# Kernel optimization log

Measured on AMD Instinct MI355X. Metric: run time of the kernel, lower is better.

## Reference

```python
import jax, jax.numpy as jnp
import numpy as np

B, S, D, H = 4, 2048, 1024, 16
DK = D // H  # 64


def setup_inputs() -> dict:
    key = jax.random.key(0)
    ks = jax.random.split(key, 7)
    scale = 1.0 / np.sqrt(D)
    q = jax.random.normal(ks[0], (B, S, D), dtype=jnp.float32)
    k = jax.random.normal(ks[1], (B, S, D), dtype=jnp.float32)
    v = jax.random.normal(ks[2], (B, S, D), dtype=jnp.float32)
    # causal mask, broadcastable to [B, H, S, S]
    mask = jnp.tril(jnp.ones((S, S), dtype=jnp.int32))[None, None, :, :]
    Wq = jax.random.normal(ks[3], (D, D), dtype=jnp.float32) * scale
    Wk = jax.random.normal(ks[4], (D, D), dtype=jnp.float32) * scale
    Wv = jax.random.normal(ks[5], (D, D), dtype=jnp.float32) * scale
    Wo = jax.random.normal(ks[6], (D, D), dtype=jnp.float32) * scale
    return {"q": q, "k": k, "v": v, "mask": mask,
            "Wq": Wq, "Wk": Wk, "Wv": Wv, "Wo": Wo}


def reference(q, k, v, mask, Wq, Wk, Wv, Wo):
    # nn.Linear(bias=False): y = x @ W.T
    query = jnp.einsum('bsd,ed->bse', q, Wq).reshape(B, S, H, DK).transpose(0, 2, 1, 3)
    key_ = jnp.einsum('bsd,ed->bse', k, Wk).reshape(B, S, H, DK).transpose(0, 2, 1, 3)
    value = jnp.einsum('bsd,ed->bse', v, Wv).reshape(B, S, H, DK).transpose(0, 2, 1, 3)
    scores = jnp.einsum('bhqd,bhkd->bhqk', query, key_) / jnp.sqrt(jnp.float32(DK))
    scores = jnp.where(mask == 0, -jnp.inf, scores)
    probs = jax.nn.softmax(scores, axis=-1)
    x = jnp.einsum('bhqk,bhkd->bhqd', probs, value)  # [B,H,S,DK]
    x = x.transpose(0, 2, 1, 3).reshape(B, S, D)
    return jnp.einsum('bsd,ed->bse', x, Wo)
```

## Files before the change

### kernel.cpp

```cpp
#include <hip/hip_runtime.h>
#include <hip/hip_bf16.h>

constexpr int Bn = 4, Sn = 2048, Dn = 1024, Hn = 16, DKn = 64;
constexpr int Mrows = Bn * Sn;
constexpr int NQB = Sn / 64;

typedef __attribute__((ext_vector_type(8))) short short8;
typedef __attribute__((ext_vector_type(4))) float f32x4;
typedef __attribute__((ext_vector_type(4))) unsigned int u32x4;

#define DEV __device__ __forceinline__

DEV unsigned short f2bf(float f) {
    unsigned u = __builtin_bit_cast(unsigned, f);
    u += 0x7FFFu + ((u >> 16) & 1u);
    return (unsigned short)(u >> 16);
}
DEV unsigned pk2(float a, float b) {
    __hip_bfloat162 h = __float22bfloat162_rn(float2{a, b});
    unsigned u;
    __builtin_memcpy(&u, &h, 4);
    return u;
}
DEV float exp2a(float x) {
    float r;
    asm("v_exp_f32 %0, %1" : "=v"(r) : "v"(x));
    return r;
}

__global__ __launch_bounds__(256) void cvt_w(const float* __restrict__ W0,
                                             const float* __restrict__ W1,
                                             const float* __restrict__ W2,
                                             const float* __restrict__ W3,
                                             unsigned short* __restrict__ Out) {
    const float* src = blockIdx.y == 0 ? W0
                     : blockIdx.y == 1 ? W1
                     : blockIdx.y == 2 ? W2 : W3;
    size_t off = ((size_t)blockIdx.x * 256 + threadIdx.x) * 8;
    const float4* s = (const float4*)(src + off);
    float4 a = s[0], b = s[1];
    u32x4 p = {pk2(a.x, a.y), pk2(a.z, a.w), pk2(b.x, b.y), pk2(b.z, b.w)};
    *(u32x4*)(Out + (size_t)blockIdx.y * (Dn * Dn) + off) = p;
}

template <bool ABF16, bool BBF16, bool OUTF32>
DEV void gemm_body(const void* __restrict__ Ap, const void* __restrict__ Bw,
                   void* __restrict__ Out) {
    __shared__ alignas(16) unsigned short As[128 * 40];
    __shared__ alignas(16) unsigned short Bs[128 * 40];

    const int tid = threadIdx.x;
    const int bid = (int)(blockIdx.y * gridDim.x + blockIdx.x);
    const int xcd = bid & 7;
    const int jj = bid >> 3;
    const int m0 = (xcd + ((jj & 7) << 3)) * 128;
    const int n0 = (jj >> 3) * 128;
    const int lane = tid & 63;
    const int w = tid >> 6;
    const int wm = (w >> 1) * 32;
    const int wn = (w & 1) * 64;
    const int g = lane >> 4, q15 = lane & 15;

    f32x4 acc[2][4] = {};

    const int srow = tid >> 2, sseg = tid & 3;

    const float* Af = (const float*)Ap;
    const unsigned short* Ab = (const unsigned short*)Ap;
    const float* Bf = (const float*)Bw;
    const unsigned short* Bb = (const unsigned short*)Bw;

    float4 fa0, fa1, fb0, fb1;
    u32x4 ua0, ub0;

    auto loadA = [&](int kk) {
        if constexpr (ABF16) {
            ua0 = *(const u32x4*)(Ab + (size_t)(m0 + srow) * Dn + kk + sseg * 8);
        } else {
            const float4* s =
                (const float4*)(Af + (size_t)(m0 + srow) * Dn + kk + sseg * 8);
            fa0 = s[0];
            fa1 = s[1];
        }
    };
    auto loadB = [&](int kk) {
        if constexpr (BBF16) {
            ub0 = *(const u32x4*)(Bb + (size_t)(n0 + srow) * Dn + kk + sseg * 8);
        } else {
            const float4* s =
                (const float4*)(Bf + (size_t)(n0 + srow) * Dn + kk + sseg * 8);
            fb0 = s[0];
            fb1 = s[1];
        }
    };
    auto store = [&]() {
        u32x4* da = (u32x4*)(&As[srow * 40 + sseg * 8]);
        if constexpr (ABF16) {
            da[0] = ua0;
        } else {
            u32x4 p0 = {pk2(fa0.x, fa0.y), pk2(fa0.z, fa0.w), pk2(fa1.x, fa1.y),
                        pk2(fa1.z, fa1.w)};
            da[0] = p0;
        }
        u32x4* db = (u32x4*)(&Bs[srow * 40 + sseg * 8]);
        if constexpr (BBF16) {
            db[0] = ub0;
        } else {
            u32x4 q0 = {pk2(fb0.x, fb0.y), pk2(fb0.z, fb0.w), pk2(fb1.x, fb1.y),
                        pk2(fb1.z, fb1.w)};
            db[0] = q0;
        }
    };

    loadA(0);
    loadB(0);
    for (int kk = 0; kk < Dn; kk += 32) {
        store();
        __syncthreads();
        if (kk + 32 < Dn) {
            loadA(kk + 32);
            loadB(kk + 32);
        }

        short8 af[2], bf[4];
#pragma unroll
        for (int mf = 0; mf < 2; ++mf)
            af[mf] = __builtin_bit_cast(
                short8, *(const u32x4*)(&As[(wm + mf * 16 + q15) * 40 + g * 8]));
#pragma unroll
        for (int nf = 0; nf < 4; ++nf)
            bf[nf] = __builtin_bit_cast(
                short8, *(const u32x4*)(&Bs[(wn + nf * 16 + q15) * 40 + g * 8]));
#pragma unroll
        for (int mf = 0; mf < 2; ++mf)
#pragma unroll
            for (int nf = 0; nf < 4; ++nf)
                acc[mf][nf] = __builtin_amdgcn_mfma_f32_16x16x32_bf16(
                    af[mf], bf[nf], acc[mf][nf], 0, 0, 0);
        __syncthreads();
    }

#pragma unroll
    for (int mf = 0; mf < 2; ++mf)
#pragma unroll
        for (int nf = 0; nf < 4; ++nf)
#pragma unroll
            for (int r = 0; r < 4; ++r) {
                int m = m0 + wm + mf * 16 + 4 * g + r;
                int n = n0 + wn + nf * 16 + q15;
                float val = acc[mf][nf][r];
                if (OUTF32) {
                    ((float*)Out)[(size_t)m * Dn + n] = val;
                } else {
                    int b = m >> 11, s = m & (Sn - 1);
                    int h = n >> 6, dk = n & 63;
                    ((unsigned short*)Out)[(((size_t)(b * Hn + h) * Sn + s) << 6) +
                                           dk] = f2bf(val);
                }
            }
}

template <bool ABF16, bool BBF16, bool OUTF32>
__global__ __launch_bounds__(512) void gemm_nt(const void* __restrict__ Ap,
                                               const void* __restrict__ Bw,
                                               void* __restrict__ Out) {
    gemm_body<ABF16, BBF16, OUTF32>(Ap, Bw, Out);
}

__global__ __launch_bounds__(256) void attn_fwd(
    const unsigned short* __restrict__ Qb, const unsigned short* __restrict__ Kb,
    const unsigned short* __restrict__ Vb, unsigned short* __restrict__ Xb) {
    __shared__ alignas(16) unsigned short Kt[64 * 64];
    __shared__ alignas(16) unsigned short Vt[64 * 64];

    constexpr float SCL = 0.18033688f;

    const int tid = threadIdx.x;
    const int pair = blockIdx.x;
    const int bh = blockIdx.y;
    const int b = bh >> 4, h = bh & 15;
    const int lane = tid & 63, w = tid >> 6;
    const int g = lane >> 4, q15 = lane & 15;

    const unsigned short* Qh = Qb + (size_t)bh * Sn * DKn;
    const unsigned short* Kh = Kb + (size_t)bh * Sn * DKn;
    const unsigned short* Vh = Vb + (size_t)bh * Sn * DKn;

    const int st_row = tid >> 2, st_seg = tid & 3;
    const int sv_kv = tid & 63, sv_g = tid >> 6;
    const int sel = sv_kv & 1;
    const int kv_even = sv_kv & ~1;
    const unsigned kvp = (unsigned)(((kv_even & 32) | ((kv_even & 12) << 1) |
                                     ((kv_even & 16) >> 2) | (kv_even & 3)) *
                                    2);

    const short8 ones = {0x3F80, 0x3F80, 0x3F80, 0x3F80,
                         0x3F80, 0x3F80, 0x3F80, 0x3F80};

    u32x4 kr0, kr1, vr0, vr1;
    auto load_kv = [&](int j) {
        kr0 = *(const u32x4*)(Kh + (size_t)(j * 64 + st_row) * DKn + st_seg * 8);
        kr1 = *(const u32x4*)(Kh + (size_t)(j * 64 + st_row) * DKn +
                              (st_seg + 4) * 8);
        vr0 = *(const u32x4*)(Vh + (size_t)(j * 64 + sv_kv) * DKn + sv_g * 8);
        vr1 = *(const u32x4*)(Vh + (size_t)(j * 64 + sv_kv) * DKn + sv_g * 8 + 32);
    };

    for (int hp = 0; hp < 2; ++hp) {
        const int qblk = hp == 0 ? (NQB - 1 - pair) : pair;
        const int qg = qblk * 64 + w * 16 + q15;

        short8 qf[2];
#pragma unroll
        for (int ks = 0; ks < 2; ++ks)
            qf[ks] = __builtin_bit_cast(
                short8, *(const u32x4*)(Qh + (size_t)qg * DKn + ks * 32 + g * 8));

        f32x4 xacc[4] = {};
        f32x4 xl = {};
        float m_run = -1e30f;

        load_kv(0);
        for (int j = 0; j <= qblk; ++j) {
            {
                unsigned b0 = ((unsigned)(st_row * 128 + st_seg * 16)) ^
                              ((unsigned)(st_row & 7) << 4);
                unsigned b1 = ((unsigned)(st_row * 128 + (st_seg + 4) * 16)) ^
                              ((unsigned)(st_row & 7) << 4);
                *(u32x4*)((char*)Kt + b0) = kr0;
                *(u32x4*)((char*)Kt + b1) = kr1;
            }
#pragma unroll
            for (int r2 = 0; r2 < 2; ++r2) {
                u32x4 vvec = r2 ? vr1 : vr0;
                int dk0 = sv_g * 8 + r2 * 32;
#pragma unroll
                for (int i = 0; i < 4; ++i) {
                    unsigned mine = vvec[i];
                    unsigned theirs = (unsigned)__shfl_xor((int)mine, 1);
                    int dk_abs = dk0 + 2 * i + sel;
                    unsigned out = sel ? ((theirs >> 16) | (mine & 0xffff0000u))
                                       : ((mine & 0xffffu) | (theirs << 16));
                    unsigned byteoff = ((unsigned)(dk_abs * 128) + kvp) ^
                                       ((unsigned)(dk_abs & 7) << 4);
                    *(unsigned*)((char*)Vt + byteoff) = out;
                }
            }
            __syncthreads();

            if (j < qblk) load_kv(j + 1);

            f32x4 sacc[4] = {};
#pragma unroll
            for (int mf = 0; mf < 4; ++mf) {
                int row = mf * 16 + q15;
#pragma unroll
                for (int ks = 0; ks < 2; ++ks) {
                    unsigned byteoff = ((unsigned)(row * 128 + ks * 64 + g * 16)) ^
                                       ((unsigned)(row & 7) << 4);
                    short8 kf = __builtin_bit_cast(
                        short8, *(const u32x4*)((char*)Kt + byteoff));
                    sacc[mf] = __builtin_amdgcn_mfma_f32_16x16x32_bf16(
                        kf, qf[ks], sacc[mf], 0, 0, 0);
                }
            }

            float p[4][4];
            float pmax = -1e30f;
            const bool diag = (j == qblk);
#pragma unroll
            for (int mf = 0; mf < 4; ++mf)
#pragma unroll
                for (int r = 0; r < 4; ++r) {
                    float sv = sacc[mf][r];
                    if (diag) {
                        int kvg = j * 64 + mf * 16 + 4 * g + r;
                        if (kvg > qg) sv = -1e30f;
                    }
                    p[mf][r] = sv;
                    pmax = fmaxf(pmax, sv);
                }
            pmax = fmaxf(pmax, __shfl_xor(pmax, 16));
            pmax = fmaxf(pmax, __shfl_xor(pmax, 32));
            float pmax_s = pmax * SCL;
            if (__any(pmax_s > m_run + 8.f)) {
                float mnew = fmaxf(m_run, pmax_s);
                float corr = exp2a(m_run - mnew);
#pragma unroll
                for (int mf = 0; mf < 4; ++mf)
#pragma unroll
                    for (int r = 0; r < 4; ++r) xacc[mf][r] *= corr;
#pragma unroll
                for (int r = 0; r < 4; ++r) xl[r] *= corr;
                m_run = mnew;
            }
#pragma unroll
            for (int mf = 0; mf < 4; ++mf)
#pragma unroll
                for (int r = 0; r < 4; ++r)
                    p[mf][r] = exp2a(p[mf][r] * SCL - m_run);

            unsigned pkk[4][2];
#pragma unroll
            for (int mf = 0; mf < 4; ++mf) {
                pkk[mf][0] = pk2(p[mf][0], p[mf][1]);
                pkk[mf][1] = pk2(p[mf][2], p[mf][3]);
            }
#pragma unroll
            for (int ks = 0; ks < 2; ++ks) {
                u32x4 tmp = {pkk[2 * ks][0], pkk[2 * ks][1], pkk[2 * ks + 1][0],
                             pkk[2 * ks + 1][1]};
                short8 pb = __builtin_bit_cast(short8, tmp);
                xl = __builtin_amdgcn_mfma_f32_16x16x32_bf16(ones, pb, xl, 0, 0, 0);
#pragma unroll
                for (int mf = 0; mf < 4; ++mf) {
                    int row = mf * 16 + q15;
                    unsigned byteoff = ((unsigned)(row * 128 + ks * 64 + g * 16)) ^
                                       ((unsigned)(row & 7) << 4);
                    short8 vf = __builtin_bit_cast(
                        short8, *(const u32x4*)((char*)Vt + byteoff));
                    xacc[mf] = __builtin_amdgcn_mfma_f32_16x16x32_bf16(
                        vf, pb, xacc[mf], 0, 0, 0);
                }
            }
            __syncthreads();
        }

        float inv = 1.0f / xl[0];
        size_t rowbase = (size_t)(b * Sn + qblk * 64 + w * 16 + q15) * Dn + h * 64;
#pragma unroll
        for (int mf = 0; mf < 4; ++mf) {
            unsigned w0 = pk2(xacc[mf][0] * inv, xacc[mf][1] * inv);
            unsigned w1 = pk2(xacc[mf][2] * inv, xacc[mf][3] * inv);
            uint2 val = {w0, w1};
            *(uint2*)(Xb + rowbase + mf * 16 + 4 * g) = val;
        }
    }
}

extern "C" void kernel_launch(void* const* d_in, const int* in_sizes, int n_in,
                              void* d_out, int out_size, void* d_ws, size_t ws_size,
                              hipStream_t stream) {
    (void)in_sizes; (void)n_in; (void)out_size;
    const float* q = (const float*)d_in[0];
    const float* k = (const float*)d_in[1];
    const float* v = (const float*)d_in[2];
    const float* Wq = (const float*)d_in[4];
    const float* Wk = (const float*)d_in[5];
    const float* Wv = (const float*)d_in[6];
    const float* Wo = (const float*)d_in[7];

    unsigned short* Qb = (unsigned short*)d_ws;
    unsigned short* Kb = Qb + (size_t)Mrows * Dn;
    unsigned short* Vb = Kb + (size_t)Mrows * Dn;
    unsigned short* Xb = Vb + (size_t)Mrows * Dn;
    unsigned short* Wb = Xb + (size_t)Mrows * Dn;

    const size_t needW =
        (size_t)4 * Mrows * Dn * 2 + (size_t)4 * Dn * Dn * 2;
    const bool useWb = ws_size >= needW;

    dim3 blk(256);
    dim3 gblk(512);
    dim3 ggrid(Dn / 128, Mrows / 128);

    if (useWb) {
        cvt_w<<<dim3(Dn * Dn / (256 * 8), 4), blk, 0, stream>>>(Wq, Wk, Wv, Wo, Wb);
        const unsigned short* Wqb = Wb;
        const unsigned short* Wkb = Wb + (size_t)Dn * Dn;
        const unsigned short* Wvb = Wb + (size_t)2 * Dn * Dn;
        const unsigned short* Wob = Wb + (size_t)3 * Dn * Dn;
        gemm_nt<false, true, false><<<ggrid, gblk, 0, stream>>>(q, Wqb, Qb);
        gemm_nt<false, true, false><<<ggrid, gblk, 0, stream>>>(k, Wkb, Kb);
        gemm_nt<false, true, false><<<ggrid, gblk, 0, stream>>>(v, Wvb, Vb);
        attn_fwd<<<dim3(NQB / 2, Bn * Hn), blk, 0, stream>>>(Qb, Kb, Vb, Xb);
        gemm_nt<true, true, true><<<ggrid, gblk, 0, stream>>>(Xb, Wob, d_out);
    } else {
        gemm_nt<false, false, false><<<ggrid, gblk, 0, stream>>>(q, Wq, Qb);
        gemm_nt<false, false, false><<<ggrid, gblk, 0, stream>>>(k, Wk, Kb);
        gemm_nt<false, false, false><<<ggrid, gblk, 0, stream>>>(v, Wv, Vb);
        attn_fwd<<<dim3(NQB / 2, Bn * Hn), blk, 0, stream>>>(Qb, Kb, Vb, Xb);
        gemm_nt<true, false, true><<<ggrid, gblk, 0, stream>>>(Xb, Wo, d_out);
    }
}
```

Baseline: 220.1 us.

## Widen attention blocks to 128 query rows sharing each K/V tile

The attention kernel now runs 512 threads (8 waves) per block, each block covering 128 query rows instead of 64. Every K/V tile staged in LDS is shared by twice as many waves, and each thread loads half as much per tile. Waves in the lower half skip the compute for the last KV tile past their causal diagonal but still join the barriers. This halves the grid to 8x64 blocks and adds some idle time at barriers for the first four waves on the final tile.

```diff
diff --git a/kernel.cpp b/kernel.cpp
--- a/kernel.cpp
+++ b/kernel.cpp
@@ -167,7 +167,7 @@
     gemm_body<ABF16, BBF16, OUTF32>(Ap, Bw, Out);
 }
 
-__global__ __launch_bounds__(256) void attn_fwd(
+__global__ __launch_bounds__(512) void attn_fwd(
     const unsigned short* __restrict__ Qb, const unsigned short* __restrict__ Kb,
     const unsigned short* __restrict__ Vb, unsigned short* __restrict__ Xb) {
     __shared__ alignas(16) unsigned short Kt[64 * 64];
@@ -186,7 +186,7 @@
     const unsigned short* Kh = Kb + (size_t)bh * Sn * DKn;
     const unsigned short* Vh = Vb + (size_t)bh * Sn * DKn;
 
-    const int st_row = tid >> 2, st_seg = tid & 3;
+    const int st_row = tid >> 3, st_seg = tid & 7;
     const int sv_kv = tid & 63, sv_g = tid >> 6;
     const int sel = sv_kv & 1;
     const int kv_even = sv_kv & ~1;
@@ -197,18 +197,17 @@
     const short8 ones = {0x3F80, 0x3F80, 0x3F80, 0x3F80,
                          0x3F80, 0x3F80, 0x3F80, 0x3F80};
 
-    u32x4 kr0, kr1, vr0, vr1;
+    u32x4 kr0, vr0;
     auto load_kv = [&](int j) {
         kr0 = *(const u32x4*)(Kh + (size_t)(j * 64 + st_row) * DKn + st_seg * 8);
-        kr1 = *(const u32x4*)(Kh + (size_t)(j * 64 + st_row) * DKn +
-                              (st_seg + 4) * 8);
         vr0 = *(const u32x4*)(Vh + (size_t)(j * 64 + sv_kv) * DKn + sv_g * 8);
-        vr1 = *(const u32x4*)(Vh + (size_t)(j * 64 + sv_kv) * DKn + sv_g * 8 + 32);
     };
 
     for (int hp = 0; hp < 2; ++hp) {
-        const int qblk = hp == 0 ? (NQB - 1 - pair) : pair;
-        const int qg = qblk * 64 + w * 16 + q15;
+        const int c = hp == 0 ? (15 - pair) : pair;
+        const int jmax = 2 * c + 1;
+        const int jdiag = 2 * c + (w >> 2);
+        const int qg = c * 128 + w * 16 + q15;
 
         short8 qf[2];
 #pragma unroll
@@ -221,22 +220,17 @@
         float m_run = -1e30f;
 
         load_kv(0);
-        for (int j = 0; j <= qblk; ++j) {
+        for (int j = 0; j <= jmax; ++j) {
             {
                 unsigned b0 = ((unsigned)(st_row * 128 + st_seg * 16)) ^
                               ((unsigned)(st_row & 7) << 4);
-                unsigned b1 = ((unsigned)(st_row * 128 + (st_seg + 4) * 16)) ^
-                              ((unsigned)(st_row & 7) << 4);
                 *(u32x4*)((char*)Kt + b0) = kr0;
-                *(u32x4*)((char*)Kt + b1) = kr1;
             }
-#pragma unroll
-            for (int r2 = 0; r2 < 2; ++r2) {
-                u32x4 vvec = r2 ? vr1 : vr0;
-                int dk0 = sv_g * 8 + r2 * 32;
+            {
+                int dk0 = sv_g * 8;
 #pragma unroll
                 for (int i = 0; i < 4; ++i) {
-                    unsigned mine = vvec[i];
+                    unsigned mine = vr0[i];
                     unsigned theirs = (unsigned)__shfl_xor((int)mine, 1);
                     int dk_abs = dk0 + 2 * i + sel;
                     unsigned out = sel ? ((theirs >> 16) | (mine & 0xffff0000u))
@@ -248,86 +242,91 @@
             }
             __syncthreads();
 
-            if (j < qblk) load_kv(j + 1);
-
-            f32x4 sacc[4] = {};
-#pragma unroll
-            for (int mf = 0; mf < 4; ++mf) {
-                int row = mf * 16 + q15;
-#pragma unroll
-                for (int ks = 0; ks < 2; ++ks) {
-                    unsigned byteoff = ((unsigned)(row * 128 + ks * 64 + g * 16)) ^
-                                       ((unsigned)(row & 7) << 4);
-                    short8 kf = __builtin_bit_cast(
-                        short8, *(const u32x4*)((char*)Kt + byteoff));
-                    sacc[mf] = __builtin_amdgcn_mfma_f32_16x16x32_bf16(
-                        kf, qf[ks], sacc[mf], 0, 0, 0);
-                }
-            }
-
-            float p[4][4];
-            float pmax = -1e30f;
-            const bool diag = (j == qblk);
-#pragma unroll
-            for (int mf = 0; mf < 4; ++mf)
-#pragma unroll
-                for (int r = 0; r < 4; ++r) {
-                    float sv = sacc[mf][r];
-                    if (diag) {
-                        int kvg = j * 64 + mf * 16 + 4 * g + r;
-                        if (kvg > qg) sv = -1e30f;
-                    }
-                    p[mf][r] = sv;
-                    pmax = fmaxf(pmax, sv);
-                }
-            pmax = fmaxf(pmax, __shfl_xor(pmax, 16));
-            pmax = fmaxf(pmax, __shfl_xor(pmax, 32));
-            float pmax_s = pmax * SCL;
-            if (__any(pmax_s > m_run + 8.f)) {
-                float mnew = fmaxf(m_run, pmax_s);
-                float corr = exp2a(m_run - mnew);
-#pragma unroll
-                for (int mf = 0; mf < 4; ++mf)
-#pragma unroll
-                    for (int r = 0; r < 4; ++r) xacc[mf][r] *= corr;
-#pragma unroll
-                for (int r = 0; r < 4; ++r) xl[r] *= corr;
-                m_run = mnew;
-            }
-#pragma unroll
-            for (int mf = 0; mf < 4; ++mf)
-#pragma unroll
-                for (int r = 0; r < 4; ++r)
-                    p[mf][r] = exp2a(p[mf][r] * SCL - m_run);
-
-            unsigned pkk[4][2];
-#pragma unroll
-            for (int mf = 0; mf < 4; ++mf) {
-                pkk[mf][0] = pk2(p[mf][0], p[mf][1]);
-                pkk[mf][1] = pk2(p[mf][2], p[mf][3]);
-            }
-#pragma unroll
-            for (int ks = 0; ks < 2; ++ks) {
-                u32x4 tmp = {pkk[2 * ks][0], pkk[2 * ks][1], pkk[2 * ks + 1][0],
-                             pkk[2 * ks + 1][1]};
-                short8 pb = __builtin_bit_cast(short8, tmp);
-                xl = __builtin_amdgcn_mfma_f32_16x16x32_bf16(ones, pb, xl, 0, 0, 0);
+            if (j < jmax) load_kv(j + 1);
+
+            if (j <= jdiag) {
+                f32x4 sacc[4] = {};
 #pragma unroll
                 for (int mf = 0; mf < 4; ++mf) {
                     int row = mf * 16 + q15;
-                    unsigned byteoff = ((unsigned)(row * 128 + ks * 64 + g * 16)) ^
-                                       ((unsigned)(row & 7) << 4);
-                    short8 vf = __builtin_bit_cast(
-                        short8, *(const u32x4*)((char*)Vt + byteoff));
-                    xacc[mf] = __builtin_amdgcn_mfma_f32_16x16x32_bf16(
-                        vf, pb, xacc[mf], 0, 0, 0);
+#pragma unroll
+                    for (int ks = 0; ks < 2; ++ks) {
+                        unsigned byteoff =
+                            ((unsigned)(row * 128 + ks * 64 + g * 16)) ^
+                            ((unsigned)(row & 7) << 4);
+                        short8 kf = __builtin_bit_cast(
+                            short8, *(const u32x4*)((char*)Kt + byteoff));
+                        sacc[mf] = __builtin_amdgcn_mfma_f32_16x16x32_bf16(
+                            kf, qf[ks], sacc[mf], 0, 0, 0);
+                    }
+                }
+
+                float p[4][4];
+                float pmax = -1e30f;
+                const bool diag = (j == jdiag);
+#pragma unroll
+                for (int mf = 0; mf < 4; ++mf)
+#pragma unroll
+                    for (int r = 0; r < 4; ++r) {
+                        float sv = sacc[mf][r];
+                        if (diag) {
+                            int kvg = j * 64 + mf * 16 + 4 * g + r;
+                            if (kvg > qg) sv = -1e30f;
+                        }
+                        p[mf][r] = sv;
+                        pmax = fmaxf(pmax, sv);
+                    }
+                pmax = fmaxf(pmax, __shfl_xor(pmax, 16));
+                pmax = fmaxf(pmax, __shfl_xor(pmax, 32));
+                float pmax_s = pmax * SCL;
+                if (__any(pmax_s > m_run + 8.f)) {
+                    float mnew = fmaxf(m_run, pmax_s);
+                    float corr = exp2a(m_run - mnew);
+#pragma unroll
+                    for (int mf = 0; mf < 4; ++mf)
+#pragma unroll
+                        for (int r = 0; r < 4; ++r) xacc[mf][r] *= corr;
+#pragma unroll
+                    for (int r = 0; r < 4; ++r) xl[r] *= corr;
+                    m_run = mnew;
+                }
+#pragma unroll
+                for (int mf = 0; mf < 4; ++mf)
+#pragma unroll
+                    for (int r = 0; r < 4; ++r)
+                        p[mf][r] = exp2a(p[mf][r] * SCL - m_run);
+
+                unsigned pkk[4][2];
+#pragma unroll
+                for (int mf = 0; mf < 4; ++mf) {
+                    pkk[mf][0] = pk2(p[mf][0], p[mf][1]);
+                    pkk[mf][1] = pk2(p[mf][2], p[mf][3]);
+                }
+#pragma unroll
+                for (int ks = 0; ks < 2; ++ks) {
+                    u32x4 tmp = {pkk[2 * ks][0], pkk[2 * ks][1],
+                                 pkk[2 * ks + 1][0], pkk[2 * ks + 1][1]};
+                    short8 pb = __builtin_bit_cast(short8, tmp);
+                    xl = __builtin_amdgcn_mfma_f32_16x16x32_bf16(ones, pb, xl,
+                                                                 0, 0, 0);
+#pragma unroll
+                    for (int mf = 0; mf < 4; ++mf) {
+                        int row = mf * 16 + q15;
+                        unsigned byteoff =
+                            ((unsigned)(row * 128 + ks * 64 + g * 16)) ^
+                            ((unsigned)(row & 7) << 4);
+                        short8 vf = __builtin_bit_cast(
+                            short8, *(const u32x4*)((char*)Vt + byteoff));
+                        xacc[mf] = __builtin_amdgcn_mfma_f32_16x16x32_bf16(
+                            vf, pb, xacc[mf], 0, 0, 0);
+                    }
                 }
             }
             __syncthreads();
         }
 
         float inv = 1.0f / xl[0];
-        size_t rowbase = (size_t)(b * Sn + qblk * 64 + w * 16 + q15) * Dn + h * 64;
+        size_t rowbase = (size_t)(b * Sn + c * 128 + w * 16 + q15) * Dn + h * 64;
 #pragma unroll
         for (int mf = 0; mf < 4; ++mf) {
             unsigned w0 = pk2(xacc[mf][0] * inv, xacc[mf][1] * inv);
@@ -363,6 +362,7 @@
     dim3 blk(256);
     dim3 gblk(512);
     dim3 ggrid(Dn / 128, Mrows / 128);
+    dim3 agrid(NQB / 4, Bn * Hn);
 
     if (useWb) {
         cvt_w<<<dim3(Dn * Dn / (256 * 8), 4), blk, 0, stream>>>(Wq, Wk, Wv, Wo, Wb);
@@ -373,13 +373,13 @@
         gemm_nt<false, true, false><<<ggrid, gblk, 0, stream>>>(q, Wqb, Qb);
         gemm_nt<false, true, false><<<ggrid, gblk, 0, stream>>>(k, Wkb, Kb);
         gemm_nt<false, true, false><<<ggrid, gblk, 0, stream>>>(v, Wvb, Vb);
-        attn_fwd<<<dim3(NQB / 2, Bn * Hn), blk, 0, stream>>>(Qb, Kb, Vb, Xb);
+        attn_fwd<<<agrid, gblk, 0, stream>>>(Qb, Kb, Vb, Xb);
         gemm_nt<true, true, true><<<ggrid, gblk, 0, stream>>>(Xb, Wob, d_out);
     } else {
         gemm_nt<false, false, false><<<ggrid, gblk, 0, stream>>>(q, Wq, Qb);
         gemm_nt<false, false, false><<<ggrid, gblk, 0, stream>>>(k, Wk, Kb);
         gemm_nt<false, false, false><<<ggrid, gblk, 0, stream>>>(v, Wv, Vb);
-        attn_fwd<<<dim3(NQB / 2, Bn * Hn), blk, 0, stream>>>(Qb, Kb, Vb, Xb);
+        attn_fwd<<<agrid, gblk, 0, stream>>>(Qb, Kb, Vb, Xb);
         gemm_nt<true, false, true><<<ggrid, gblk, 0, stream>>>(Xb, Wo, d_out);
     }
 }
```

Result: faster. 202.6 us (-7.9%).
